# Kernel tuning notes

Measured on AMD Instinct MI355X. Metric: run time of the kernel, lower is better.

The kernel has to match this reference:

```python
import jax, jax.numpy as jnp
import numpy as np

TEMP = 30.0  # softmax temperature from init kwarg
NUM_EXPERTS = 4


def setup_inputs() -> dict:
    key = jax.random.key(0)
    ks = jax.random.split(key, 4)
    B, Cin, H, W = 32, 128, 56, 56
    Cout, K, E, R = 256, 3, NUM_EXPERTS, 16  # R = max(Cin//reduction, reduction)
    x = jax.random.normal(ks[0], (B, Cin, H, W), dtype=jnp.float32)
    # expert conv bank: torch.rand -> uniform[0,1)
    convs = jax.random.uniform(ks[1], (E, Cout, Cin, K, K), dtype=jnp.float32)
    # router MLP (nn.Linear has bias by default)
    w1 = jax.random.normal(ks[2], (R, Cin), dtype=jnp.float32) * 0.05
    b1 = jnp.zeros((R,), dtype=jnp.float32)
    w2 = jax.random.normal(ks[3], (E, R), dtype=jnp.float32) * 0.05
    b2 = jnp.zeros((E,), dtype=jnp.float32)
    return {"x": x, "convs": convs, "w1": w1, "b1": b1, "w2": w2, "b2": b2}


def reference(x, convs, w1, b1, w2, b2):
    B, Cin, H, W = x.shape
    E, Cout, _, K, _ = convs.shape
    # per-sample global average pool -> router MLP -> softmax(logits / temp)
    gap = x.mean(axis=(2, 3))                      # [B, Cin]
    h = jax.nn.relu(gap @ w1.T + b1)               # [B, R]
    logits = h @ w2.T + b2                         # [B, E]
    routing = jax.nn.softmax(logits / TEMP, axis=-1)
    # per-sample mixed conv kernels [B, Cout, Cin, K, K]
    kern = jnp.einsum('be,eoikl->boikl', routing, convs)
    # batched per-sample conv via grouped conv: treat batch as groups
    xg = x.reshape(1, B * Cin, H, W)
    kg = kern.reshape(B * Cout, Cin, K, K)
    out = jax.lax.conv_general_dilated(
        xg, kg,
        window_strides=(1, 1),
        padding=[(1, 1), (1, 1)],
        feature_group_count=B,
        dimension_numbers=('NCHW', 'OIHW', 'NCHW'))
    return out.reshape(B, Cout, out.shape[2], out.shape[3])
```

## Files before the change

kernel.cpp:

```cpp
#include <hip/hip_runtime.h>
#include <hip/hip_bf16.h>

#define NB   32
#define CIN  128
#define HH   56
#define WW   56
#define COUT 256
#define HW   3136
#define NCHUNK 576

typedef __bf16 bf16x8 __attribute__((ext_vector_type(8)));
typedef float floatx4 __attribute__((ext_vector_type(4)));

__global__ void router_kernel(const float* __restrict__ gpart,
                              const float* __restrict__ w1, const float* __restrict__ b1,
                              const float* __restrict__ w2, const float* __restrict__ b2,
                              float* __restrict__ routing) {
    int b = blockIdx.x, ch = threadIdx.x;
    __shared__ float gs[CIN];
    __shared__ float hs[16];
    float s = 0.f;
    #pragma unroll 7
    for (int hwb = 0; hwb < 49; ++hwb)
        s += gpart[((size_t)b * 49 + hwb) * CIN + ch];
    gs[ch] = s * (1.0f / HW);
    __syncthreads();
    if (ch < 16) {
        float a = 0.f;
        #pragma unroll
        for (int i = 0; i < CIN; ++i) a += gs[i] * w1[ch * CIN + i];
        hs[ch] = fmaxf(a + b1[ch], 0.f);
    }
    __syncthreads();
    if (ch == 0) {
        float lg[4], mx = -1e30f;
        #pragma unroll
        for (int e = 0; e < 4; ++e) {
            float a = b2[e];
            #pragma unroll
            for (int r = 0; r < 16; ++r) a += hs[r] * w2[e * 16 + r];
            lg[e] = a * (1.0f / 30.0f);
            mx = fmaxf(mx, lg[e]);
        }
        float den = 0.f, ex[4];
        #pragma unroll
        for (int e = 0; e < 4; ++e) { ex[e] = expf(lg[e] - mx); den += ex[e]; }
        #pragma unroll
        for (int e = 0; e < 4; ++e) routing[b * 4 + e] = ex[e] / den;
    }
}

__global__ void xpose_wswz(const float* __restrict__ x, __hip_bfloat16* __restrict__ xT,
                           float* __restrict__ gpart,
                           const float* __restrict__ convs, __hip_bfloat16* __restrict__ convT) {
    __shared__ __align__(16) char smem[19008];
    int blk = blockIdx.x;
    if (blk < 3136) {
        int hwb = blk % 49; int rem = blk / 49; int ih = rem & 1; int b = rem >> 1;
        int hw0 = hwb * 64, i0 = ih * 64;
        float (*tile)[65] = (float(*)[65])smem;
        float (*red)[4]   = (float(*)[4])(smem + 16640);
        const float* xp = x + ((size_t)b * CIN + i0) * HW + hw0;
        for (int t = threadIdx.x; t < 1024; t += 256) {
            int ir = t >> 4, c4 = t & 15;
            float4 v = *(const float4*)(xp + (size_t)ir * HW + c4 * 4);
            tile[ir][c4 * 4 + 0] = v.x; tile[ir][c4 * 4 + 1] = v.y;
            tile[ir][c4 * 4 + 2] = v.z; tile[ir][c4 * 4 + 3] = v.w;
        }
        __syncthreads();
        __hip_bfloat16* op = xT + ((size_t)b * HW + hw0) * CIN + i0;
        for (int t = threadIdx.x; t < 512; t += 256) {
            int pp = t >> 3, seg = t & 7;
            __hip_bfloat16 tmp[8];
            #pragma unroll
            for (int j = 0; j < 8; ++j) tmp[j] = __float2bfloat16(tile[seg * 8 + j][pp]);
            *(uint4*)(op + (size_t)pp * CIN + seg * 8) = *(uint4*)tmp;
        }
        int ch = threadIdx.x & 63, grp = threadIdx.x >> 6;
        float s = 0.f;
        #pragma unroll
        for (int k = 0; k < 16; ++k) s += tile[ch][grp * 16 + k];
        red[ch][grp] = s;
        __syncthreads();
        if (threadIdx.x < 64) {
            float t4 = red[threadIdx.x][0] + red[threadIdx.x][1]
                     + red[threadIdx.x][2] + red[threadIdx.x][3];
            gpart[((size_t)b * 49 + blk % 49) * CIN + i0 + threadIdx.x] = t4;
        }
    } else {
        int b2 = blk - 3136;
        int ks = b2 & 1, cc = (b2 >> 1) & 1, mt = (b2 >> 2) & 3;
        int wm = (b2 >> 4) & 1, mtile = (b2 >> 5) & 1, e = b2 >> 6;
        float (*tl)[297] = (float(*)[297])smem;
        int row0 = mtile * 128 + wm * 64 + mt * 16;
        const float* src = convs + (size_t)(e * COUT + row0) * 1152 + (cc * 64 + ks * 32) * 9;
        for (int i = threadIdx.x; i < 1152; i += 256) {
            int r = i / 72, o = i - r * 72;
            float4 v = *(const float4*)(src + (size_t)r * 1152 + o * 4);
            tl[r][o * 4 + 0] = v.x; tl[r][o * 4 + 1] = v.y;
            tl[r][o * 4 + 2] = v.z; tl[r][o * 4 + 3] = v.w;
        }
        __syncthreads();
        for (int i = threadIdx.x; i < 576; i += 256) {
            int p = i >> 6, lane = i & 63;
            int col = lane & 15, quad = lane >> 4;
            int c = mtile * 288 + p * 32 + cc * 16 + ks * 8 + mt * 2 + wm;
            __hip_bfloat16 tmp[8];
            #pragma unroll
            for (int j = 0; j < 8; ++j)
                tmp[j] = __float2bfloat16(tl[col][(quad * 8 + j) * 9 + p]);
            *(uint4*)(convT + ((size_t)(e * NCHUNK + c) * 64 + lane) * 8) = *(uint4*)tmp;
        }
    }
}

__global__ void mix_kernel(const __hip_bfloat16* __restrict__ convT,
                           const float* __restrict__ routing,
                           __hip_bfloat16* __restrict__ wmix) {
    int t = blockIdx.x * 256 + threadIdx.x;
    const int PER_B = NCHUNK * 32;
    int b = t / PER_B;
    int p = t - b * PER_B;
    float r0 = routing[b * 4 + 0], r1 = routing[b * 4 + 1];
    float r2 = routing[b * 4 + 2], r3 = routing[b * 4 + 3];
    const size_t ES = (size_t)NCHUNK * 64 * 8;
    const __hip_bfloat16* sp = convT + (size_t)p * 16;
    __hip_bfloat16 o[16];
    #pragma unroll
    for (int h = 0; h < 2; ++h) {
        bf16x8 w0 = *(const bf16x8*)(sp + h * 8);
        bf16x8 w1 = *(const bf16x8*)(sp + h * 8 + ES);
        bf16x8 w2 = *(const bf16x8*)(sp + h * 8 + 2 * ES);
        bf16x8 w3 = *(const bf16x8*)(sp + h * 8 + 3 * ES);
        #pragma unroll
        for (int j = 0; j < 8; ++j) {
            float v = r0 * (float)w0[j] + r1 * (float)w1[j]
                    + r2 * (float)w2[j] + r3 * (float)w3[j];
            o[h * 8 + j] = __float2bfloat16(v);
        }
    }
    uint4* d = (uint4*)(wmix + (size_t)t * 16);
    d[0] = ((uint4*)o)[0];
    d[1] = ((uint4*)o)[1];
}

#define XSTRIDE 136
__global__ __launch_bounds__(256, 2)
void conv_mfma(const __hip_bfloat16* __restrict__ xT,
               const __hip_bfloat16* __restrict__ wmix,
               float* __restrict__ out) {
    __shared__ __align__(16) __hip_bfloat16 xs[180 * XSTRIDE];

    int lin = blockIdx.x;
    int wg  = (lin & 7) * 224 + (lin >> 3);
    int b   = wg / 56;
    int rr  = wg - b * 56;
    int mtile = rr / 28;
    int tile  = rr - mtile * 28;

    const int yt = tile >> 2, xt = tile & 3;
    const int y0 = yt * 8, x0 = xt * 16;
    const int tid = threadIdx.x;
    const int lane = tid & 63, wave = tid >> 6;
    const int wm = wave & 1, wn = wave >> 1;
    const int col = lane & 15, quad = lane >> 4;

    const __hip_bfloat16* xb = xT + (size_t)b * HW * CIN;
    const __hip_bfloat16* wptr = wmix +
        ((size_t)(b * NCHUNK + mtile * 288 + wm)) * 512 + lane * 8;

    #pragma unroll
    for (int j = 0; j < 12; ++j) {
        int tt = tid + j * 256;
        if (tt < 2880) {
            int pix = tt >> 4, seg = tt & 15;
            int py = pix / 18, px = pix - py * 18;
            int gy = y0 - 1 + py, gx = x0 - 1 + px;
            uint4 v = {0u, 0u, 0u, 0u};
            if ((unsigned)gy < 56u && (unsigned)gx < 56u)
                v = *(const uint4*)(xb + ((size_t)(gy * 56 + gx) * CIN + seg * 8));
            *(uint4*)(&xs[pix * XSTRIDE + seg * 8]) = v;
        }
    }

    floatx4 acc[4][4];
    #pragma unroll
    for (int mt = 0; mt < 4; ++mt)
        #pragma unroll
        for (int nt = 0; nt < 4; ++nt)
            acc[mt][nt] = (floatx4){0.f, 0.f, 0.f, 0.f};

    bf16x8 af[4][4];
    bf16x8 bfr[2][6];

    auto lda = [&](int u, bf16x8* dst) {
        const int g = u / 3, ky = u - g * 3;
        const int cc = g / 6, r6 = g - cc * 6;
        const int ks = r6 / 3, kx = r6 - ks * 3;
        const int pp = ky * 3 + kx;
        #pragma unroll
        for (int mt = 0; mt < 4; ++mt)
            dst[mt] = *(const bf16x8*)(wptr +
                (size_t)(pp * 32 + cc * 16 + ks * 8 + mt * 2) * 512);
    };
    auto ldb = [&](int g, bf16x8* dst) {
        const int cc = g / 6, r6 = g - cc * 6;
        const int ks = r6 / 3, kx = r6 - ks * 3;
        const int base = cc * 64 + ks * 32 + quad * 8;
        #pragma unroll
        for (int r = 0; r < 6; ++r)
            dst[r] = *(const bf16x8*)(&xs[((wn * 4 + r) * 18 + col + kx) * XSTRIDE + base]);
    };

    lda(0, af[0]); lda(1, af[1]); lda(2, af[2]);
    __syncthreads();
    ldb(0, bfr[0]);

    #pragma unroll
    for (int g = 0; g < 12; ++g) {
        if (g + 1 < 12) ldb(g + 1, bfr[(g + 1) & 1]);
        #pragma unroll
        for (int ky = 0; ky < 3; ++ky) {
            const int u = g * 3 + ky;
            if (u + 3 < 36) lda(u + 3, af[(u + 3) & 3]);
            __builtin_amdgcn_s_setprio(1);
            #pragma unroll
            for (int mt = 0; mt < 4; ++mt)
                #pragma unroll
                for (int nt = 0; nt < 4; ++nt)
                    acc[mt][nt] = __builtin_amdgcn_mfma_f32_16x16x32_bf16(
                        af[u & 3][mt], bfr[g & 1][nt + ky], acc[mt][nt], 0, 0, 0);
            __builtin_amdgcn_s_setprio(0);
        }
    }

    const int x = x0 + col;
    if (x < 56) {
        #pragma unroll
        for (int mt = 0; mt < 4; ++mt) {
            int o = mtile * 128 + wm * 64 + mt * 16 + quad * 4;
            #pragma unroll
            for (int nt = 0; nt < 4; ++nt) {
                int y = y0 + wn * 4 + nt;
                float* op = out + (((size_t)b * COUT + o) * 56 + y) * 56 + x;
                #pragma unroll
                for (int r = 0; r < 4; ++r)
                    op[(size_t)r * HW] = acc[mt][nt][r];
            }
        }
    }
}

extern "C" void kernel_launch(void* const* d_in, const int* in_sizes, int n_in,
                              void* d_out, int out_size, void* d_ws, size_t ws_size,
                              hipStream_t stream) {
    const float* x     = (const float*)d_in[0];
    const float* convs = (const float*)d_in[1];
    const float* w1    = (const float*)d_in[2];
    const float* b1    = (const float*)d_in[3];
    const float* w2    = (const float*)d_in[4];
    const float* b2    = (const float*)d_in[5];
    float* out = (float*)d_out;

    char* ws = (char*)d_ws;
    float* routing       = (float*)(ws + 16384);
    __hip_bfloat16* xT   = (__hip_bfloat16*)(ws + 16896);
    __hip_bfloat16* wmix = (__hip_bfloat16*)(ws + 16896 + 25690112);
    __hip_bfloat16* convT= (__hip_bfloat16*)(ws + 16896 + 25690112 + 18874368);
    float* gpart = (float*)wmix;

    xpose_wswz   <<<3392, 256, 0, stream>>>(x, xT, gpart, convs, convT);
    router_kernel<<<NB, 128, 0, stream>>>(gpart, w1, b1, w2, b2, routing);
    mix_kernel   <<<2304, 256, 0, stream>>>(convT, routing, wmix);
    conv_mfma    <<<1792, 256, 0, stream>>>(xT, wmix, out);
}
```

Before: 210.9 us.

## Fuse router into mix kernel and raise conv occupancy to three waves

Removes the separate router launch. Each mix block now recomputes its sample's routing weights from the GAP partial sums, which are stored temporarily in the output buffer. The conv kernel's launch bounds go from 2 to 3 blocks per SM, and the A-fragment prefetch depth drops from 3 to 2 to cut register pressure. The trade-offs are redundant router work across the 72 blocks per sample and less latency hiding in the conv loop.

```diff
diff --git a/kernel.cpp b/kernel.cpp
--- a/kernel.cpp
+++ b/kernel.cpp
@@ -11,44 +11,6 @@
 
 typedef __bf16 bf16x8 __attribute__((ext_vector_type(8)));
 typedef float floatx4 __attribute__((ext_vector_type(4)));
-
-__global__ void router_kernel(const float* __restrict__ gpart,
-                              const float* __restrict__ w1, const float* __restrict__ b1,
-                              const float* __restrict__ w2, const float* __restrict__ b2,
-                              float* __restrict__ routing) {
-    int b = blockIdx.x, ch = threadIdx.x;
-    __shared__ float gs[CIN];
-    __shared__ float hs[16];
-    float s = 0.f;
-    #pragma unroll 7
-    for (int hwb = 0; hwb < 49; ++hwb)
-        s += gpart[((size_t)b * 49 + hwb) * CIN + ch];
-    gs[ch] = s * (1.0f / HW);
-    __syncthreads();
-    if (ch < 16) {
-        float a = 0.f;
-        #pragma unroll
-        for (int i = 0; i < CIN; ++i) a += gs[i] * w1[ch * CIN + i];
-        hs[ch] = fmaxf(a + b1[ch], 0.f);
-    }
-    __syncthreads();
-    if (ch == 0) {
-        float lg[4], mx = -1e30f;
-        #pragma unroll
-        for (int e = 0; e < 4; ++e) {
-            float a = b2[e];
-            #pragma unroll
-            for (int r = 0; r < 16; ++r) a += hs[r] * w2[e * 16 + r];
-            lg[e] = a * (1.0f / 30.0f);
-            mx = fmaxf(mx, lg[e]);
-        }
-        float den = 0.f, ex[4];
-        #pragma unroll
-        for (int e = 0; e < 4; ++e) { ex[e] = expf(lg[e] - mx); den += ex[e]; }
-        #pragma unroll
-        for (int e = 0; e < 4; ++e) routing[b * 4 + e] = ex[e] / den;
-    }
-}
 
 __global__ void xpose_wswz(const float* __restrict__ x, __hip_bfloat16* __restrict__ xT,
                            float* __restrict__ gpart,
@@ -85,7 +47,7 @@
         if (threadIdx.x < 64) {
             float t4 = red[threadIdx.x][0] + red[threadIdx.x][1]
                      + red[threadIdx.x][2] + red[threadIdx.x][3];
-            gpart[((size_t)b * 49 + blk % 49) * CIN + i0 + threadIdx.x] = t4;
+            gpart[((size_t)b * 49 + hwb) * CIN + i0 + threadIdx.x] = t4;
         }
     } else {
         int b2 = blk - 3136;
@@ -114,28 +76,69 @@
     }
 }
 
-__global__ void mix_kernel(const __hip_bfloat16* __restrict__ convT,
-                           const float* __restrict__ routing,
+__global__ void mix_router(const __hip_bfloat16* __restrict__ convT,
+                           const float* __restrict__ gpart,
+                           const float* __restrict__ w1, const float* __restrict__ b1,
+                           const float* __restrict__ w2, const float* __restrict__ b2,
                            __hip_bfloat16* __restrict__ wmix) {
-    int t = blockIdx.x * 256 + threadIdx.x;
+    __shared__ float g2[2][CIN];
+    __shared__ float gs[CIN];
+    __shared__ float hs[16];
+    __shared__ float rr[4];
+    int blk = blockIdx.x, tid = threadIdx.x;
+    int b = blk / 72;
+    {
+        int ch = tid & 127, half = tid >> 7;
+        float s = 0.f;
+        #pragma unroll 5
+        for (int h = half; h < 49; h += 2)
+            s += gpart[((size_t)b * 49 + h) * CIN + ch];
+        g2[half][ch] = s;
+        __syncthreads();
+        if (tid < CIN) gs[tid] = (g2[0][tid] + g2[1][tid]) * (1.0f / HW);
+        __syncthreads();
+        if (tid < 16) {
+            float a = 0.f;
+            #pragma unroll
+            for (int i = 0; i < CIN; ++i) a += gs[i] * w1[tid * CIN + i];
+            hs[tid] = fmaxf(a + b1[tid], 0.f);
+        }
+        __syncthreads();
+        if (tid == 0) {
+            float lg[4], mx = -1e30f;
+            #pragma unroll
+            for (int e = 0; e < 4; ++e) {
+                float a = b2[e];
+                #pragma unroll
+                for (int r = 0; r < 16; ++r) a += hs[r] * w2[e * 16 + r];
+                lg[e] = a * (1.0f / 30.0f);
+                mx = fmaxf(mx, lg[e]);
+            }
+            float den = 0.f, ex[4];
+            #pragma unroll
+            for (int e = 0; e < 4; ++e) { ex[e] = expf(lg[e] - mx); den += ex[e]; }
+            #pragma unroll
+            for (int e = 0; e < 4; ++e) rr[e] = ex[e] / den;
+        }
+        __syncthreads();
+    }
+    float r0 = rr[0], r1 = rr[1], r2 = rr[2], r3 = rr[3];
+    int t = blk * 256 + tid;
     const int PER_B = NCHUNK * 32;
-    int b = t / PER_B;
     int p = t - b * PER_B;
-    float r0 = routing[b * 4 + 0], r1 = routing[b * 4 + 1];
-    float r2 = routing[b * 4 + 2], r3 = routing[b * 4 + 3];
     const size_t ES = (size_t)NCHUNK * 64 * 8;
     const __hip_bfloat16* sp = convT + (size_t)p * 16;
     __hip_bfloat16 o[16];
     #pragma unroll
     for (int h = 0; h < 2; ++h) {
         bf16x8 w0 = *(const bf16x8*)(sp + h * 8);
-        bf16x8 w1 = *(const bf16x8*)(sp + h * 8 + ES);
-        bf16x8 w2 = *(const bf16x8*)(sp + h * 8 + 2 * ES);
-        bf16x8 w3 = *(const bf16x8*)(sp + h * 8 + 3 * ES);
+        bf16x8 w1v = *(const bf16x8*)(sp + h * 8 + ES);
+        bf16x8 w2v = *(const bf16x8*)(sp + h * 8 + 2 * ES);
+        bf16x8 w3v = *(const bf16x8*)(sp + h * 8 + 3 * ES);
         #pragma unroll
         for (int j = 0; j < 8; ++j) {
-            float v = r0 * (float)w0[j] + r1 * (float)w1[j]
-                    + r2 * (float)w2[j] + r3 * (float)w3[j];
+            float v = r0 * (float)w0[j] + r1 * (float)w1v[j]
+                    + r2 * (float)w2v[j] + r3 * (float)w3v[j];
             o[h * 8 + j] = __float2bfloat16(v);
         }
     }
@@ -145,7 +148,7 @@
 }
 
 #define XSTRIDE 136
-__global__ __launch_bounds__(256, 2)
+__global__ __launch_bounds__(256, 3)
 void conv_mfma(const __hip_bfloat16* __restrict__ xT,
                const __hip_bfloat16* __restrict__ wmix,
                float* __restrict__ out) {
@@ -190,7 +193,7 @@
         for (int nt = 0; nt < 4; ++nt)
             acc[mt][nt] = (floatx4){0.f, 0.f, 0.f, 0.f};
 
-    bf16x8 af[4][4];
+    bf16x8 af[3][4];
     bf16x8 bfr[2][6];
 
     auto lda = [&](int u, bf16x8* dst) {
@@ -212,7 +215,7 @@
             dst[r] = *(const bf16x8*)(&xs[((wn * 4 + r) * 18 + col + kx) * XSTRIDE + base]);
     };
 
-    lda(0, af[0]); lda(1, af[1]); lda(2, af[2]);
+    lda(0, af[0]); lda(1, af[1]);
     __syncthreads();
     ldb(0, bfr[0]);
 
@@ -222,14 +225,14 @@
         #pragma unroll
         for (int ky = 0; ky < 3; ++ky) {
             const int u = g * 3 + ky;
-            if (u + 3 < 36) lda(u + 3, af[(u + 3) & 3]);
+            if (u + 2 < 36) lda(u + 2, af[(u + 2) % 3]);
             __builtin_amdgcn_s_setprio(1);
             #pragma unroll
             for (int mt = 0; mt < 4; ++mt)
                 #pragma unroll
                 for (int nt = 0; nt < 4; ++nt)
                     acc[mt][nt] = __builtin_amdgcn_mfma_f32_16x16x32_bf16(
-                        af[u & 3][mt], bfr[g & 1][nt + ky], acc[mt][nt], 0, 0, 0);
+                        af[u % 3][mt], bfr[g & 1][nt + ky], acc[mt][nt], 0, 0, 0);
             __builtin_amdgcn_s_setprio(0);
         }
     }
@@ -263,14 +266,12 @@
     float* out = (float*)d_out;
 
     char* ws = (char*)d_ws;
-    float* routing       = (float*)(ws + 16384);
     __hip_bfloat16* xT   = (__hip_bfloat16*)(ws + 16896);
     __hip_bfloat16* wmix = (__hip_bfloat16*)(ws + 16896 + 25690112);
     __hip_bfloat16* convT= (__hip_bfloat16*)(ws + 16896 + 25690112 + 18874368);
-    float* gpart = (float*)wmix;
-
-    xpose_wswz   <<<3392, 256, 0, stream>>>(x, xT, gpart, convs, convT);
-    router_kernel<<<NB, 128, 0, stream>>>(gpart, w1, b1, w2, b2, routing);
-    mix_kernel   <<<2304, 256, 0, stream>>>(convT, routing, wmix);
-    conv_mfma    <<<1792, 256, 0, stream>>>(xT, wmix, out);
-}
+    float* gpart = out;
+
+    xpose_wswz <<<3392, 256, 0, stream>>>(x, xT, gpart, convs, convT);
+    mix_router <<<2304, 256, 0, stream>>>(convT, gpart, w1, b1, w2, b2, wmix);
+    conv_mfma  <<<1792, 256, 0, stream>>>(xT, wmix, out);
+}
```

After: 265.9 us. +26.1%, slower.
